# Optimization experiments

Measured on AMD Instinct MI355X. Metric: run time of the kernel, lower is better.

Reference implementation:

```python
import jax, jax.numpy as jnp
import numpy as np

EPS = 1e-5
_INV_STD = 1.0 / np.sqrt(1.0 + EPS)  # eval-mode BN with running_mean=0, running_var=1


def conv1x1(x, w):
    # x: (B,C,H,W), w: (O,C) -> (B,O,H,W)
    return jnp.einsum('bchw,oc->bohw', x, w)


def bn_relu(x, gamma, beta):
    y = x * (_INV_STD * gamma)[None, :, None, None] + beta[None, :, None, None]
    return jax.nn.relu(y)


def setup_inputs() -> dict:
    key = jax.random.key(0)
    ks = jax.random.split(key, 8)
    B, C, H, W, Kc, Kp = 8, 512, 128, 128, 256, 19
    s = 0.02
    return {
        'x': jax.random.normal(ks[0], (B, C, H, W), jnp.float32),
        'proxy_feats': jax.random.normal(ks[1], (B, C, Kp, 1), jnp.float32),
        'wq1': jax.random.normal(ks[2], (Kc, C), jnp.float32) * s,
        'gq1': jnp.ones((Kc,), jnp.float32), 'bq1': jnp.zeros((Kc,), jnp.float32),
        'wq2': jax.random.normal(ks[3], (Kc, Kc), jnp.float32) * s,
        'gq2': jnp.ones((Kc,), jnp.float32), 'bq2': jnp.zeros((Kc,), jnp.float32),
        'wk1': jax.random.normal(ks[4], (Kc, C), jnp.float32) * s,
        'gk1': jnp.ones((Kc,), jnp.float32), 'bk1': jnp.zeros((Kc,), jnp.float32),
        'wk2': jax.random.normal(ks[5], (Kc, Kc), jnp.float32) * s,
        'gk2': jnp.ones((Kc,), jnp.float32), 'bk2': jnp.zeros((Kc,), jnp.float32),
        'wv': jax.random.normal(ks[6], (Kc, C), jnp.float32) * s,
        'gv': jnp.ones((Kc,), jnp.float32), 'bv': jnp.zeros((Kc,), jnp.float32),
        'wo': jax.random.normal(ks[7], (C, Kc), jnp.float32) * s,
        'go': jnp.ones((C,), jnp.float32), 'bo': jnp.zeros((C,), jnp.float32),
    }


def reference(x, proxy_feats, wq1, gq1, bq1, wq2, gq2, bq2,
              wk1, gk1, bk1, wk2, gk2, bk2, wv, gv, bv, wo, go, bo):
    B, C, H, W = x.shape
    Kc = wq1.shape[0]
    # projections: 1x1 conv -> BN(eval) -> ReLU chains
    q = bn_relu(conv1x1(bn_relu(conv1x1(x, wq1), gq1, bq1), wq2), gq2, bq2)          # (B,Kc,H,W)
    k = bn_relu(conv1x1(bn_relu(conv1x1(proxy_feats, wk1), gk1, bk1), wk2), gk2, bk2)[..., 0]  # (B,Kc,Kp)
    v = bn_relu(conv1x1(proxy_feats, wv), gv, bv)[..., 0]                             # (B,Kc,Kp)
    qf = q.reshape(B, Kc, H * W).transpose(0, 2, 1)                                   # (B,HW,Kc)
    sim = jnp.einsum('bnc,bck->bnk', qf, k) * (Kc ** -0.5)                            # (B,HW,Kp)
    att = jax.nn.softmax(sim, axis=-1)
    ctx = jnp.einsum('bnk,bck->bnc', att, v)                                          # (B,HW,Kc)
    ctx = ctx.transpose(0, 2, 1).reshape(B, Kc, H, W)
    return bn_relu(conv1x1(ctx, wo), go, bo)                                          # (B,C,H,W)
```

## Files before the change

kernel.cpp:

```cpp
#include <hip/hip_runtime.h>

#define INV_STD 0.9999950000374997f

typedef unsigned short u16;
typedef __bf16 bf16x8 __attribute__((ext_vector_type(8)));
typedef __bf16 bf16x4 __attribute__((ext_vector_type(4)));
typedef float f32x4 __attribute__((ext_vector_type(4)));

__device__ __forceinline__ u16 f2bf(float f) {
    unsigned int u = __float_as_uint(f);
    u += 0x7fffu + ((u >> 16) & 1u);
    return (u16)(u >> 16);
}

__device__ __forceinline__ void gl_lds16(const void* g, void* l) {
    __builtin_amdgcn_global_load_lds(
        (const __attribute__((address_space(1))) unsigned int*)(unsigned long long)g,
        (__attribute__((address_space(3))) unsigned int*)(unsigned int)(unsigned long long)l,
        16, 0, 0);
}

__device__ __forceinline__ f32x4 mfma16(bf16x8 a, bf16x8 b, f32x4 c) {
    return __builtin_amdgcn_mfma_f32_16x16x32_bf16(a, b, c, 0, 0, 0);
}

__device__ __forceinline__ unsigned lds_off(const void* p) {
    return (unsigned)(unsigned long long)p;
}

__device__ __forceinline__ bf16x4 tr_read(unsigned addr) {
    bf16x4 r;
    asm volatile("ds_read_b64_tr_b16 %0, %1" : "=v"(r) : "v"(addr));
    return r;
}

__device__ __forceinline__ bf16x8 ldg8(const u16* p) {
    return *(const bf16x8*)p;
}

__global__ __launch_bounds__(256) void prep_kernel(
    const float* __restrict__ proxy,
    const float* __restrict__ wk1, const float* __restrict__ gk1, const float* __restrict__ bk1,
    const float* __restrict__ wk2, const float* __restrict__ gk2, const float* __restrict__ bk2,
    const float* __restrict__ wv,  const float* __restrict__ gv,  const float* __restrict__ bv,
    const float* __restrict__ wo,  const float* __restrict__ go,
    const float* __restrict__ wq1, const float* __restrict__ gq1,
    const float* __restrict__ wq2, const float* __restrict__ gq2,
    u16* __restrict__ KB,
    u16* __restrict__ WoVB,
    u16* __restrict__ WQ1B, u16* __restrict__ WQ2B)
{
    int blk = blockIdx.x;
    int t = threadIdx.x;
    if (blk >= 256) {
        if (blk < 768) {
            long i = (long)(blk - 256) * 256 + t;
            int o = (int)(i >> 9);
            int q = (int)(i & 511);
            int r = q & 31;
            int src = (q & ~31) + ((r >> 3) & 3) * 4 + (r & 3) + ((r >> 2) & 1) * 16;
            WQ1B[i] = f2bf(wq1[(long)o * 512 + src] * (INV_STD * gq1[o]));
        } else {
            long i = (long)(blk - 768) * 256 + t;
            int o = (int)(i >> 8);
            WQ2B[i] = f2bf(wq2[i] * (INV_STD * gq2[o]));
        }
        return;
    }
    int b = blk >> 5, p = blk & 31;
    if (p >= 19) {
        KB[((long)b * 32 + p) * 256 + t] = 0;
        WoVB[((long)b * 512 + t) * 32 + p] = 0;
        WoVB[((long)b * 512 + 256 + t) * 32 + p] = 0;
        return;
    }
    __shared__ float px[512];
    __shared__ float k1[256];
    __shared__ float vcol[256];
    for (int i = t; i < 512; i += 256) px[i] = proxy[((long)b * 512 + i) * 19 + p];
    __syncthreads();
    float aK = 0.f, aV = 0.f;
    {
        const float4* wk1r = (const float4*)(wk1 + (long)t * 512);
        const float4* wvr  = (const float4*)(wv  + (long)t * 512);
        const float4* pxv  = (const float4*)px;
        #pragma unroll 4
        for (int c = 0; c < 128; ++c) {
            float4 pv = pxv[c];
            float4 k4 = wk1r[c];
            float4 v4 = wvr[c];
            aK += k4.x * pv.x + k4.y * pv.y + k4.z * pv.z + k4.w * pv.w;
            aV += v4.x * pv.x + v4.y * pv.y + v4.z * pv.z + v4.w * pv.w;
        }
    }
    float k1v = fmaxf(aK * (INV_STD * gk1[t]) + bk1[t], 0.f);
    float vv  = fmaxf(aV * (INV_STD * gv[t])  + bv[t],  0.f);
    k1[t] = k1v;
    vcol[t] = vv;
    __syncthreads();
    {
        float a2 = 0.f;
        const float4* wk2r = (const float4*)(wk2 + (long)t * 256);
        const float4* k1v4 = (const float4*)k1;
        #pragma unroll 4
        for (int c = 0; c < 64; ++c) {
            float4 w4 = wk2r[c];
            float4 kk = k1v4[c];
            a2 += w4.x * kk.x + w4.y * kk.y + w4.z * kk.z + w4.w * kk.w;
        }
        KB[((long)b * 32 + p) * 256 + t] = f2bf(fmaxf(a2 * (INV_STD * gk2[t]) + bk2[t], 0.f));
    }
    {
        float a0 = 0.f, a1 = 0.f;
        const float4* wr0 = (const float4*)(wo + (long)t * 256);
        const float4* wr1 = (const float4*)(wo + (long)(t + 256) * 256);
        const float4* vc4 = (const float4*)vcol;
        #pragma unroll 4
        for (int c = 0; c < 64; ++c) {
            float4 v4 = vc4[c];
            float4 w0 = wr0[c];
            float4 w1 = wr1[c];
            a0 += w0.x * v4.x + w0.y * v4.y + w0.z * v4.z + w0.w * v4.w;
            a1 += w1.x * v4.x + w1.y * v4.y + w1.z * v4.z + w1.w * v4.w;
        }
        WoVB[((long)b * 512 + t) * 32 + p] = f2bf(INV_STD * go[t] * a0);
        WoVB[((long)b * 512 + 256 + t) * 32 + p] = f2bf(INV_STD * go[t + 256] * a1);
    }
}

__global__ __launch_bounds__(256, 2) void fused_all(
    const float* __restrict__ X,
    const u16* __restrict__ W1,
    const float* __restrict__ b1,
    const u16* __restrict__ W2,
    const float* __restrict__ b2,
    const u16* __restrict__ KB,
    const u16* __restrict__ WoVB,
    const float* __restrict__ obias,
    float* __restrict__ out)
{
    __shared__ __align__(16) u16 xs[64 * 64];
    __shared__ __align__(16) u16 lB[2][256 * 32];
    __shared__ __align__(16) u16 q12s[64 * 264];
    __shared__ __align__(16) u16 atts[64 * 40];
    int t = threadIdx.x, lane = t & 63, w = t >> 6;
    int l16 = lane & 15, hi = lane >> 4;
    long m0 = (long)blockIdx.x * 64;
    int b = (int)(m0 >> 14);
    int pixg = (int)(m0 & 16383);
    const float* xb = X + (long)b * 512 * 16384 + pixg;
    int ca = t >> 4;
    int aa = t & 15;
    int rW = lane >> 2;
    int cW = (lane & 3) << 3;
    unsigned trb = lds_off(&xs[hi * 64 + l16]);

    {
        f32x4 acc[4][4] = {};
        float4 xr0, xr1, xr2, xr3;
        {
            const float* p0 = xb + (long)ca * 16384 + aa * 4;
            xr0 = *(const float4*)(p0);
            xr1 = *(const float4*)(p0 + 16L * 16384);
            xr2 = *(const float4*)(p0 + 32L * 16384);
            xr3 = *(const float4*)(p0 + 48L * 16384);
        }
        #define STW(XR, P) { \
            int c = (P) * 16 + ca; \
            ushort4 u; u.x = f2bf(XR.x); u.y = f2bf(XR.y); u.z = f2bf(XR.z); u.w = f2bf(XR.w); \
            *(ushort4*)&xs[((aa >> 2) * 16 + (c >> 2)) * 64 + (c & 3) * 16 + (aa & 3) * 4] = u; }
        for (int kt = 0; kt < 8; ++kt) {
            int k0 = kt << 6;
            if (kt > 0) __syncthreads();
            STW(xr0, 0) STW(xr1, 1) STW(xr2, 2) STW(xr3, 3)
            __syncthreads();
            bf16x8 bb0[4], bb1[4];
            #pragma unroll
            for (int j = 0; j < 4; ++j) {
                const u16* wr = W1 + (long)(w * 64 + j * 16 + l16) * 512 + k0 + hi * 8;
                bb0[j] = ldg8(wr);
                bb1[j] = ldg8(wr + 32);
            }
            if (kt < 7) {
                const float* p0 = xb + (long)(k0 + 64 + ca) * 16384 + aa * 4;
                xr0 = *(const float4*)(p0);
                xr1 = *(const float4*)(p0 + 16L * 16384);
                xr2 = *(const float4*)(p0 + 32L * 16384);
                xr3 = *(const float4*)(p0 + 48L * 16384);
            }
            bf16x4 lo0[4], hh0[4], lo1[4], hh1[4];
            #pragma unroll
            for (int i = 0; i < 4; ++i) {
                unsigned a0 = trb + i * 2048;
                lo0[i] = tr_read(a0);
                hh0[i] = tr_read(a0 + 512);
            }
            #pragma unroll
            for (int i = 0; i < 4; ++i) {
                unsigned a0 = trb + i * 2048 + 1024;
                lo1[i] = tr_read(a0);
                hh1[i] = tr_read(a0 + 512);
            }
            asm volatile("s_waitcnt lgkmcnt(8)" ::: "memory");
            __builtin_amdgcn_sched_barrier(0);
            #pragma unroll
            for (int i = 0; i < 4; ++i) {
                bf16x8 a = __builtin_shufflevector(lo0[i], hh0[i], 0, 1, 2, 3, 4, 5, 6, 7);
                #pragma unroll
                for (int j = 0; j < 4; ++j)
                    acc[i][j] = mfma16(a, bb0[j], acc[i][j]);
            }
            asm volatile("s_waitcnt lgkmcnt(0)" ::: "memory");
            __builtin_amdgcn_sched_barrier(0);
            #pragma unroll
            for (int i = 0; i < 4; ++i) {
                bf16x8 a = __builtin_shufflevector(lo1[i], hh1[i], 0, 1, 2, 3, 4, 5, 6, 7);
                #pragma unroll
                for (int j = 0; j < 4; ++j)
                    acc[i][j] = mfma16(a, bb1[j], acc[i][j]);
            }
        }
        #undef STW
        #pragma unroll
        for (int j = 0; j < 4; ++j) {
            int q = w * 4 + j;
            gl_lds16(W2 + (long)(q * 16 + rW) * 256 + cW, &lB[0][q * 512]);
        }
        float bj[4];
        #pragma unroll
        for (int j = 0; j < 4; ++j) bj[j] = b1[w * 64 + j * 16 + l16];
        #pragma unroll
        for (int i = 0; i < 4; ++i)
            #pragma unroll
            for (int r = 0; r < 4; ++r) {
                int pix = i * 16 + hi * 4 + r;
                #pragma unroll
                for (int j = 0; j < 4; ++j) {
                    float v = acc[i][j][r] + bj[j];
                    q12s[pix * 264 + w * 64 + j * 16 + l16] = f2bf(fmaxf(v, 0.f));
                }
            }
    }
    __syncthreads();
    {
        f32x4 acc[4][4] = {};
        #pragma unroll
        for (int c = 0; c < 8; ++c) {
            int cur = c & 1;
            if (c < 7) {
                int k1 = (c + 1) << 5;
                #pragma unroll
                for (int j = 0; j < 4; ++j) {
                    int q = w * 4 + j;
                    gl_lds16(W2 + (long)(q * 16 + rW) * 256 + k1 + cW, &lB[cur ^ 1][q * 512]);
                }
            }
            bf16x8 a[4], bb[4];
            #pragma unroll
            for (int i = 0; i < 4; ++i)
                a[i] = *(const bf16x8*)&q12s[(i * 16 + l16) * 264 + (c << 5) + hi * 8];
            #pragma unroll
            for (int j = 0; j < 4; ++j)
                bb[j] = *(const bf16x8*)&lB[cur][(w * 64 + j * 16 + l16) * 32 + hi * 8];
            #pragma unroll
            for (int i = 0; i < 4; ++i)
                #pragma unroll
                for (int j = 0; j < 4; ++j)
                    acc[i][j] = mfma16(a[i], bb[j], acc[i][j]);
            __syncthreads();
        }
        float bj[4];
        #pragma unroll
        for (int j = 0; j < 4; ++j) bj[j] = b2[w * 64 + j * 16 + l16];
        #pragma unroll
        for (int i = 0; i < 4; ++i)
            #pragma unroll
            for (int r = 0; r < 4; ++r) {
                int pix = i * 16 + hi * 4 + r;
                #pragma unroll
                for (int j = 0; j < 4; ++j) {
                    float v = acc[i][j][r] + bj[j];
                    q12s[pix * 264 + w * 64 + j * 16 + l16] = f2bf(fmaxf(v, 0.f));
                }
            }
    }
    __syncthreads();
    {
        f32x4 s0 = {}, s1 = {};
        #pragma unroll
        for (int ks = 0; ks < 8; ++ks) {
            bf16x8 a = *(const bf16x8*)&q12s[(w * 16 + l16) * 264 + ks * 32 + hi * 8];
            bf16x8 b0 = ldg8(KB + ((long)b * 32 + l16) * 256 + ks * 32 + hi * 8);
            bf16x8 b1v = ldg8(KB + ((long)b * 32 + 16 + l16) * 256 + ks * 32 + hi * 8);
            s0 = mfma16(a, b0, s0);
            s1 = mfma16(a, b1v, s1);
        }
        const float scale = 0.0625f;
        #pragma unroll
        for (int r = 0; r < 4; ++r) {
            float v0 = s0[r] * scale;
            float v1 = s1[r] * scale;
            float mx = fmaxf(v0, v1);
            mx = fmaxf(mx, __shfl_xor(mx, 1));
            mx = fmaxf(mx, __shfl_xor(mx, 2));
            mx = fmaxf(mx, __shfl_xor(mx, 4));
            mx = fmaxf(mx, __shfl_xor(mx, 8));
            float e0 = __expf(v0 - mx);
            float e1 = (l16 < 3) ? __expf(v1 - mx) : 0.f;
            float s = e0 + e1;
            s += __shfl_xor(s, 1);
            s += __shfl_xor(s, 2);
            s += __shfl_xor(s, 4);
            s += __shfl_xor(s, 8);
            float inv = 1.f / s;
            int pix = w * 16 + hi * 4 + r;
            atts[pix * 40 + l16] = f2bf(e0 * inv);
            atts[pix * 40 + 16 + l16] = (l16 < 3) ? f2bf(e1 * inv) : (u16)0;
        }
    }
    __syncthreads();
    {
        bf16x8 av[4], bv[8];
        #pragma unroll
        for (int mf = 0; mf < 4; ++mf)
            av[mf] = *(const bf16x8*)&atts[(mf * 16 + l16) * 40 + hi * 8];
        #pragma unroll
        for (int nf = 0; nf < 8; ++nf)
            bv[nf] = ldg8(WoVB + ((long)b * 512 + w * 128 + nf * 16 + l16) * 32 + hi * 8);
        #pragma unroll
        for (int nf = 0; nf < 8; ++nf) {
            int ch = w * 128 + nf * 16 + l16;
            float bc = obias[ch];
            float* orow = out + ((long)b * 512 + ch) * 16384 + pixg;
            #pragma unroll
            for (int mf = 0; mf < 4; ++mf) {
                f32x4 acc = mfma16(av[mf], bv[nf], (f32x4){0.f, 0.f, 0.f, 0.f});
                float4 v;
                v.x = fmaxf(acc[0] + bc, 0.f);
                v.y = fmaxf(acc[1] + bc, 0.f);
                v.z = fmaxf(acc[2] + bc, 0.f);
                v.w = fmaxf(acc[3] + bc, 0.f);
                *(float4*)&orow[mf * 16 + hi * 4] = v;
            }
        }
    }
}

extern "C" void kernel_launch(void* const* d_in, const int* in_sizes, int n_in,
                              void* d_out, int out_size, void* d_ws, size_t ws_size,
                              hipStream_t stream) {
    const float* x    = (const float*)d_in[0];
    const float* prox = (const float*)d_in[1];
    const float* wq1  = (const float*)d_in[2];
    const float* gq1  = (const float*)d_in[3];
    const float* bq1  = (const float*)d_in[4];
    const float* wq2  = (const float*)d_in[5];
    const float* gq2  = (const float*)d_in[6];
    const float* bq2  = (const float*)d_in[7];
    const float* wk1  = (const float*)d_in[8];
    const float* gk1  = (const float*)d_in[9];
    const float* bk1  = (const float*)d_in[10];
    const float* wk2  = (const float*)d_in[11];
    const float* gk2  = (const float*)d_in[12];
    const float* bk2  = (const float*)d_in[13];
    const float* wv   = (const float*)d_in[14];
    const float* gv   = (const float*)d_in[15];
    const float* bv   = (const float*)d_in[16];
    const float* wo   = (const float*)d_in[17];
    const float* go   = (const float*)d_in[18];
    const float* bo   = (const float*)d_in[19];
    float* out = (float*)d_out;

    char* ws = (char*)d_ws;
    u16* KB   = (u16*)(ws);
    u16* WoVB = (u16*)(ws + 131072);
    u16* WQ1B = (u16*)(ws + 393216);
    u16* WQ2B = (u16*)(ws + 655360);

    prep_kernel<<<1024, 256, 0, stream>>>(prox, wk1, gk1, bk1, wk2, gk2, bk2, wv, gv, bv,
                                          wo, go, wq1, gq1, wq2, gq2, KB, WoVB, WQ1B, WQ2B);
    fused_all<<<2048, 256, 0, stream>>>(x, WQ1B, bq1, WQ2B, bq2, KB, WoVB, bo, out);
}
```

Baseline: 225.1 us.

## Load X directly from global into MFMA operands, dropping LDS staging

The first projection GEMM no longer stages X through shared memory with a bf16 conversion and transpose reads. Each wave now loads its X operand straight from global memory with strided scalar loads and converts it to bf16 in registers. The W1 prepack permutation is removed to match. This removes the LDS round trip and two block barriers per k-step. In exchange every wave redundantly reads the same X tile, using scalar 4-byte strided loads with no software prefetch, which raises global and L2 traffic.

New measurement: 273.5 us. 1.21x slower.

```diff
diff --git a/kernel.cpp b/kernel.cpp
--- a/kernel.cpp
+++ b/kernel.cpp
@@ -4,7 +4,6 @@
 
 typedef unsigned short u16;
 typedef __bf16 bf16x8 __attribute__((ext_vector_type(8)));
-typedef __bf16 bf16x4 __attribute__((ext_vector_type(4)));
 typedef float f32x4 __attribute__((ext_vector_type(4)));
 
 __device__ __forceinline__ u16 f2bf(float f) {
@@ -22,16 +21,6 @@
 
 __device__ __forceinline__ f32x4 mfma16(bf16x8 a, bf16x8 b, f32x4 c) {
     return __builtin_amdgcn_mfma_f32_16x16x32_bf16(a, b, c, 0, 0, 0);
-}
-
-__device__ __forceinline__ unsigned lds_off(const void* p) {
-    return (unsigned)(unsigned long long)p;
-}
-
-__device__ __forceinline__ bf16x4 tr_read(unsigned addr) {
-    bf16x4 r;
-    asm volatile("ds_read_b64_tr_b16 %0, %1" : "=v"(r) : "v"(addr));
-    return r;
 }
 
 __device__ __forceinline__ bf16x8 ldg8(const u16* p) {
@@ -56,10 +45,7 @@
         if (blk < 768) {
             long i = (long)(blk - 256) * 256 + t;
             int o = (int)(i >> 9);
-            int q = (int)(i & 511);
-            int r = q & 31;
-            int src = (q & ~31) + ((r >> 3) & 3) * 4 + (r & 3) + ((r >> 2) & 1) * 16;
-            WQ1B[i] = f2bf(wq1[(long)o * 512 + src] * (INV_STD * gq1[o]));
+            WQ1B[i] = f2bf(wq1[i] * (INV_STD * gq1[o]));
         } else {
             long i = (long)(blk - 768) * 256 + t;
             int o = (int)(i >> 8);
@@ -139,7 +125,6 @@
     const float* __restrict__ obias,
     float* __restrict__ out)
 {
-    __shared__ __align__(16) u16 xs[64 * 64];
     __shared__ __align__(16) u16 lB[2][256 * 32];
     __shared__ __align__(16) u16 q12s[64 * 264];
     __shared__ __align__(16) u16 atts[64 * 40];
@@ -149,78 +134,34 @@
     int b = (int)(m0 >> 14);
     int pixg = (int)(m0 & 16383);
     const float* xb = X + (long)b * 512 * 16384 + pixg;
-    int ca = t >> 4;
-    int aa = t & 15;
     int rW = lane >> 2;
     int cW = (lane & 3) << 3;
-    unsigned trb = lds_off(&xs[hi * 64 + l16]);
 
     {
         f32x4 acc[4][4] = {};
-        float4 xr0, xr1, xr2, xr3;
-        {
-            const float* p0 = xb + (long)ca * 16384 + aa * 4;
-            xr0 = *(const float4*)(p0);
-            xr1 = *(const float4*)(p0 + 16L * 16384);
-            xr2 = *(const float4*)(p0 + 32L * 16384);
-            xr3 = *(const float4*)(p0 + 48L * 16384);
-        }
-        #define STW(XR, P) { \
-            int c = (P) * 16 + ca; \
-            ushort4 u; u.x = f2bf(XR.x); u.y = f2bf(XR.y); u.z = f2bf(XR.z); u.w = f2bf(XR.w); \
-            *(ushort4*)&xs[((aa >> 2) * 16 + (c >> 2)) * 64 + (c & 3) * 16 + (aa & 3) * 4] = u; }
+        #pragma unroll
         for (int kt = 0; kt < 8; ++kt) {
             int k0 = kt << 6;
-            if (kt > 0) __syncthreads();
-            STW(xr0, 0) STW(xr1, 1) STW(xr2, 2) STW(xr3, 3)
-            __syncthreads();
-            bf16x8 bb0[4], bb1[4];
-            #pragma unroll
-            for (int j = 0; j < 4; ++j) {
-                const u16* wr = W1 + (long)(w * 64 + j * 16 + l16) * 512 + k0 + hi * 8;
-                bb0[j] = ldg8(wr);
-                bb1[j] = ldg8(wr + 32);
-            }
-            if (kt < 7) {
-                const float* p0 = xb + (long)(k0 + 64 + ca) * 16384 + aa * 4;
-                xr0 = *(const float4*)(p0);
-                xr1 = *(const float4*)(p0 + 16L * 16384);
-                xr2 = *(const float4*)(p0 + 32L * 16384);
-                xr3 = *(const float4*)(p0 + 48L * 16384);
-            }
-            bf16x4 lo0[4], hh0[4], lo1[4], hh1[4];
-            #pragma unroll
-            for (int i = 0; i < 4; ++i) {
-                unsigned a0 = trb + i * 2048;
-                lo0[i] = tr_read(a0);
-                hh0[i] = tr_read(a0 + 512);
-            }
-            #pragma unroll
-            for (int i = 0; i < 4; ++i) {
-                unsigned a0 = trb + i * 2048 + 1024;
-                lo1[i] = tr_read(a0);
-                hh1[i] = tr_read(a0 + 512);
-            }
-            asm volatile("s_waitcnt lgkmcnt(8)" ::: "memory");
-            __builtin_amdgcn_sched_barrier(0);
-            #pragma unroll
-            for (int i = 0; i < 4; ++i) {
-                bf16x8 a = __builtin_shufflevector(lo0[i], hh0[i], 0, 1, 2, 3, 4, 5, 6, 7);
+            #pragma unroll
+            for (int kk = 0; kk < 2; ++kk) {
+                int kc = k0 + kk * 32 + hi * 8;
+                bf16x8 bb[4];
                 #pragma unroll
                 for (int j = 0; j < 4; ++j)
-                    acc[i][j] = mfma16(a, bb0[j], acc[i][j]);
-            }
-            asm volatile("s_waitcnt lgkmcnt(0)" ::: "memory");
-            __builtin_amdgcn_sched_barrier(0);
-            #pragma unroll
-            for (int i = 0; i < 4; ++i) {
-                bf16x8 a = __builtin_shufflevector(lo1[i], hh1[i], 0, 1, 2, 3, 4, 5, 6, 7);
-                #pragma unroll
-                for (int j = 0; j < 4; ++j)
-                    acc[i][j] = mfma16(a, bb1[j], acc[i][j]);
-            }
-        }
-        #undef STW
+                    bb[j] = ldg8(W1 + (long)(w * 64 + j * 16 + l16) * 512 + kc);
+                #pragma unroll
+                for (int i = 0; i < 4; ++i) {
+                    const float* xp = xb + (long)kc * 16384 + i * 16 + l16;
+                    bf16x8 a;
+                    #pragma unroll
+                    for (int e = 0; e < 8; ++e)
+                        a[e] = (__bf16)xp[(long)e * 16384];
+                    #pragma unroll
+                    for (int j = 0; j < 4; ++j)
+                        acc[i][j] = mfma16(a, bb[j], acc[i][j]);
+                }
+            }
+        }
         #pragma unroll
         for (int j = 0; j < 4; ++j) {
             int q = w * 4 + j;
```
